# Optimization experiments

Measured on AMD Instinct MI355X. Metric: run time of the kernel, lower is better.

The kernel has to match this reference:

```python
import jax, jax.numpy as jnp
import numpy as np

METRIC = [1, 1, 1, 1, -1]  # Cl(4,1) signature (+,+,+,+,-)


def _cayley_table():
    """32x32x32 geometric-product table for Cl(4,1); exactly one nonzero per (i,j)."""
    T = np.zeros((32, 32, 32), dtype=np.float32)
    for i in range(32):
        for j in range(32):
            k = i ^ j
            sign = 1.0
            bits = [b for b in range(5) if (i >> b) & 1] + [b for b in range(5) if (j >> b) & 1]
            swaps = 0
            for _ in range(len(bits)):
                for idx in range(len(bits) - 1):
                    if bits[idx] > bits[idx + 1]:
                        bits[idx], bits[idx + 1] = bits[idx + 1], bits[idx]
                        swaps += 1
            if swaps % 2 == 1:
                sign = -sign
            common = i & j
            for b in range(5):
                if (common >> b) & 1:
                    sign *= METRIC[b]
            T[i, j, k] = sign
    return T


def _mnorm(v, eps=1e-8):
    # stabilized L2 normalization over the last (blade) axis
    return v / (jnp.linalg.norm(v, axis=-1, keepdims=True) + eps)


def setup_inputs() -> dict:
    key = jax.random.key(0)
    k1, k2, k3, k4, k5 = jax.random.split(key, 5)
    B, T, D = 128, 512, 64
    x = jax.random.randint(k1, (B, T), 0, 4)
    emb = jax.random.normal(k2, (4, 32), dtype=jnp.float32) * 0.1
    emb = emb.at[:, 0].set(1.0)  # torch init: weight[:,0] = 1
    gin = 32 + D * 32
    gate_w = jax.random.normal(k3, (D, gin), dtype=jnp.float32) / np.sqrt(gin)
    gate_b = jnp.ones((D,), dtype=jnp.float32)  # torch init: bias.fill_(1.0)
    w1 = jax.random.normal(k4, (128, D * 32), dtype=jnp.float32) / np.sqrt(D * 32)
    b1 = jnp.zeros((128,), dtype=jnp.float32)
    ln_g = jnp.ones((128,), dtype=jnp.float32)
    ln_b = jnp.zeros((128,), dtype=jnp.float32)
    w2 = jax.random.normal(k5, (2, 128), dtype=jnp.float32) / np.sqrt(128)
    b2 = jnp.zeros((2,), dtype=jnp.float32)
    gp_table = jnp.asarray(_cayley_table())
    return {"x": x, "emb": emb, "gate_w": gate_w, "gate_b": gate_b,
            "w1": w1, "b1": b1, "ln_g": ln_g, "ln_b": ln_b,
            "w2": w2, "b2": b2, "gp_table": gp_table}


def reference(x, emb, gate_w, gate_b, w1, b1, ln_g, ln_b, w2, b2, gp_table):
    B, T = x.shape
    D = gate_b.shape[0]
    r_in = _mnorm(emb[x])  # [B,T,32]
    h0 = jnp.zeros((B, D, 32), dtype=emb.dtype).at[:, :, 0].set(1.0)

    def step(h, r_t):
        # r_t: [B,32], h: [B,D,32]
        gate_in = jnp.concatenate([h.reshape(B, D * 32), r_t], axis=-1)
        g = jax.nn.sigmoid(gate_in @ gate_w.T + gate_b)[..., None]  # [B,D,1]
        h_next = jnp.einsum('bi,bdj,ijk->bdk', r_t, h, gp_table)   # geometric product
        h = _mnorm((1.0 - g) * h + g * h_next)
        return h, None

    h, _ = jax.lax.scan(step, h0, jnp.swapaxes(r_in, 0, 1))
    z = h.reshape(B, D * 32) @ w1.T + b1
    mu = jnp.mean(z, axis=-1, keepdims=True)
    var = jnp.var(z, axis=-1, keepdims=True)
    z = (z - mu) / jnp.sqrt(var + 1e-5) * ln_g + ln_b  # LayerNorm(128)
    return jax.nn.relu(z) @ w2.T + b2  # [B,2]
```

## Files before the change

kernel.cpp:

```cpp
#include <hip/hip_runtime.h>
#include <hip/hip_fp16.h>

typedef unsigned int u32;
typedef _Float16 h2f __attribute__((ext_vector_type(2)));

#define BB 128
#define TT 512
#define DD 64
#define NBL 32
#define GIN 2080

template <int CTRL>
__device__ __forceinline__ float dpp_mov_f(float x) {
  return __builtin_bit_cast(
      float, __builtin_amdgcn_update_dpp(0, __builtin_bit_cast(int, x), CTRL,
                                         0xF, 0xF, true));
}
template <int CTRL>
__device__ __forceinline__ float dpp_add_f(float x) {
  return x + dpp_mov_f<CTRL>(x);
}
__device__ __forceinline__ float4 dpp_mov_f4_x1(float4 v) {
  return make_float4(dpp_mov_f<0xB1>(v.x), dpp_mov_f<0xB1>(v.y),
                     dpp_mov_f<0xB1>(v.z), dpp_mov_f<0xB1>(v.w));
}
__device__ __forceinline__ float swz_add16(float x) {
  return x + __builtin_bit_cast(float, __builtin_amdgcn_ds_swizzle(
                                           __builtin_bit_cast(int, x), 0x401F));
}
__device__ __forceinline__ float bpermf(int addr, float x) {
  return __builtin_bit_cast(
      float, __builtin_amdgcn_ds_bpermute(addr, __builtin_bit_cast(int, x)));
}
__device__ __forceinline__ float xorf(float a, u32 m) {
  return __builtin_bit_cast(float, __builtin_bit_cast(u32, a) ^ m);
}
__device__ __forceinline__ float uni_f(float v) {
  return __builtin_bit_cast(
      float, __builtin_amdgcn_readfirstlane(__builtin_bit_cast(int, v)));
}
__device__ __forceinline__ int uni_i(int v) {
  return __builtin_amdgcn_readfirstlane(v);
}

__device__ inline int gp_negbit(int i, int j) {
  int sw = 0;
#pragma unroll
  for (int b = 0; b < 5; ++b)
    if ((j >> b) & 1) sw += __popc(i >> (b + 1));
  return (sw ^ ((i & j) >> 4)) & 1;
}

__device__ inline float fdot2f(u32 a, u32 b, float acc) {
#if __has_builtin(__builtin_amdgcn_fdot2)
  return __builtin_amdgcn_fdot2(__builtin_bit_cast(h2f, a),
                                __builtin_bit_cast(h2f, b), acc, false);
#else
  h2f av = __builtin_bit_cast(h2f, a), bv = __builtin_bit_cast(h2f, b);
  return acc + (float)av.x * (float)bv.x + (float)av.y * (float)bv.y;
#endif
}

__device__ inline u32 pkf16(float a, float b) {
  return __builtin_bit_cast(u32, __builtin_amdgcn_cvt_pkrtz(a, b));
}

#define STEP(P, RNR, XI)                                                      \
  do {                                                                        \
    const int pn = (P) ^ 1;                                                   \
            \
    const u32* Hb = &h16t[(P)][s >> 1][(s & 1) << 5];                         \
    float a0 = 0.f, a1 = 0.f, a2 = 0.f, a3 = 0.f;                             \
    _Pragma("unroll") for (int jq = 0; jq < 8; ++jq) {                        \
      uint4 hv = *(const uint4*)(Hb + (jq << 2));                             \
      a0 = fdot2f(gw[0][4 * jq + 0], hv.x, a0);                               \
      a0 = fdot2f(gw[0][4 * jq + 1], hv.y, a0);                               \
      a0 = fdot2f(gw[0][4 * jq + 2], hv.z, a0);                               \
      a0 = fdot2f(gw[0][4 * jq + 3], hv.w, a0);                               \
      a1 = fdot2f(gw[1][4 * jq + 0], hv.x, a1);                               \
      a1 = fdot2f(gw[1][4 * jq + 1], hv.y, a1);                               \
      a1 = fdot2f(gw[1][4 * jq + 2], hv.z, a1);                               \
      a1 = fdot2f(gw[1][4 * jq + 3], hv.w, a1);                               \
      a2 = fdot2f(gw[2][4 * jq + 0], hv.x, a2);                               \
      a2 = fdot2f(gw[2][4 * jq + 1], hv.y, a2);                               \
      a2 = fdot2f(gw[2][4 * jq + 2], hv.z, a2);                               \
      a2 = fdot2f(gw[2][4 * jq + 3], hv.w, a2);                               \
      a3 = fdot2f(gw[3][4 * jq + 0], hv.x, a3);                               \
      a3 = fdot2f(gw[3][4 * jq + 1], hv.y, a3);                               \
      a3 = fdot2f(gw[3][4 * jq + 2], hv.z, a3);                               \
      a3 = fdot2f(gw[3][4 * jq + 3], hv.w, a3);                               \
    }                                                                         \
    a0 = dpp_add_f<0xB1>(a0); a0 = dpp_add_f<0x4E>(a0);                       \
    a0 = dpp_add_f<0x141>(a0); a0 = dpp_add_f<0x140>(a0); a0 = swz_add16(a0); \
    a1 = dpp_add_f<0xB1>(a1); a1 = dpp_add_f<0x4E>(a1);                       \
    a1 = dpp_add_f<0x141>(a1); a1 = dpp_add_f<0x140>(a1); a1 = swz_add16(a1); \
    a2 = dpp_add_f<0xB1>(a2); a2 = dpp_add_f<0x4E>(a2);                       \
    a2 = dpp_add_f<0x141>(a2); a2 = dpp_add_f<0x140>(a2); a2 = swz_add16(a2); \
    a3 = dpp_add_f<0xB1>(a3); a3 = dpp_add_f<0x4E>(a3);                       \
    a3 = dpp_add_f<0x141>(a3); a3 = dpp_add_f<0x140>(a3); a3 = swz_add16(a3); \
    const int jsel = rl & 3;                                                  \
    float zv = (jsel == 0) ? a0 : (jsel == 1) ? a1 : (jsel == 2) ? a2 : a3;   \
    float rcsel = ((XI) == 0)   ? rcv0                                        \
                  : ((XI) == 1) ? rcv1                                        \
                  : ((XI) == 2) ? rcv2                                        \
                                : rcv3;                                       \
    float invsel = ((XI) == 0)   ? iv0                                        \
                   : ((XI) == 1) ? iv1                                        \
                   : ((XI) == 2) ? iv2                                        \
                                 : iv3;                                       \
    float g = 1.f / (1.f + exp2f(-1.44269504f * (zv + rcsel)));               \
                  \
    float4 hq[8];                                                             \
    hq[0] = make_float4(u0, u1, u2, u3);                                      \
    hq[2] = *(const float4*)&h32[(P)][d][(2 ^ c) << 2];                       \
    hq[4] = *(const float4*)&h32[(P)][d][(4 ^ c) << 2];                       \
    hq[6] = *(const float4*)&h32[(P)][d][(6 ^ c) << 2];                       \
    hq[1] = dpp_mov_f4_x1(hq[0]);                                             \
    hq[3] = dpp_mov_f4_x1(hq[2]);                                             \
    hq[5] = dpp_mov_f4_x1(hq[4]);                                             \
    hq[7] = dpp_mov_f4_x1(hq[6]);                                             \
    float b0 = 0.f, b1v = 0.f, b2v = 0.f, b3v = 0.f;                          \
    _Pragma("unroll") for (int q = 0; q < 8; ++q) {                           \
      float t0 = xorf(RNR[q], sb[q]);                                         \
      float t1 = xorf(RNR[q + 8], sb[q + 8]);                                 \
      float t2 = xorf(RNR[q + 16], sb[q + 16]);                               \
      float t3 = xorf(RNR[q + 24], sb[q + 24]);                               \
      b0 = fmaf(t0, hq[q].x, b0);                                             \
      b1v = fmaf(t0, hq[q].y, b1v);                                           \
      b2v = fmaf(t0, hq[q].z, b2v);                                           \
      b3v = fmaf(t0, hq[q].w, b3v);                                           \
      b0 = fmaf(t1, hq[q].y, b0);                                             \
      b1v = fmaf(t1, hq[q].x, b1v);                                           \
      b2v = fmaf(t1, hq[q].w, b2v);                                           \
      b3v = fmaf(t1, hq[q].z, b3v);                                           \
      b0 = fmaf(t2, hq[q].z, b0);                                             \
      b1v = fmaf(-t2, hq[q].w, b1v);                                          \
      b2v = fmaf(-t2, hq[q].x, b2v);                                          \
      b3v = fmaf(t2, hq[q].y, b3v);                                           \
      b0 = fmaf(t3, hq[q].w, b0);                                             \
      b1v = fmaf(-t3, hq[q].z, b1v);                                          \
      b2v = fmaf(-t3, hq[q].y, b2v);                                          \
      b3v = fmaf(t3, hq[q].x, b3v);                                           \
    }                                                                         \
       \
    float gi = g * invsel;                                                    \
    float om = 1.f - g;                                                       \
    float nu0 = fmaf(gi, b0, om * hq[0].x);                                   \
    float nu1 = fmaf(gi, b1v, om * hq[0].y);                                  \
    float nu2 = fmaf(gi, b2v, om * hq[0].z);                                  \
    float nu3 = fmaf(gi, b3v, om * hq[0].w);                                  \
    float sq = nu0 * nu0 + nu1 * nu1 + nu2 * nu2 + nu3 * nu3;                 \
    sq = dpp_add_f<0xB1>(sq);                                                 \
    sq = dpp_add_f<0x4E>(sq);                                                 \
    sq = dpp_add_f<0x141>(sq);                                                \
    float sc = 1.f / (sqrtf(sq) + 1e-8f);                                     \
    u0 = nu0 * sc; u1 = nu1 * sc; u2 = nu2 * sc; u3 = nu3 * sc;               \
    *(float4*)&h32[pn][d][c << 2] = make_float4(u0, u1, u2, u3);              \
    float v0 = dpp_mov_f<0xB1>(u0);                                           \
    float v1 = dpp_mov_f<0xB1>(u1);                                           \
    float v2 = dpp_mov_f<0xB1>(u2);                                           \
    float v3 = dpp_mov_f<0xB1>(u3);                                           \
    if (!(l & 1)) {                                 \
      h16t[pn][(c) >> 1][d] = pkf16(u0, v0);                                  \
      h16t[pn][(c + 8) >> 1][d] = pkf16(u1, v1);                              \
      h16t[pn][(c + 16) >> 1][d] = pkf16(u2, v2);                             \
      h16t[pn][(c + 24) >> 1][d] = pkf16(u3, v3);                             \
    }                                                                         \
    __syncthreads();                                                          \
  } while (0)

__global__ __launch_bounds__(512, 2) void versor_fused(
    const int* __restrict__ x, const float* __restrict__ emb,
    const float* __restrict__ gate_w, const float* __restrict__ gate_b,
    const float* __restrict__ w1, const float* __restrict__ b1g,
    const float* __restrict__ ln_g, const float* __restrict__ ln_b,
    const float* __restrict__ w2, const float* __restrict__ b2,
    float* __restrict__ out) {
  __shared__ float rn[4][NBL];
  __shared__ float inv_lds[4];
  __shared__ float rc[4][DD];
  __shared__ __align__(16) float h32[2][DD][36];
  __shared__ __align__(16) u32 h16t[2][16][68];
  __shared__ __align__(16) float hs[2048];
  __shared__ float redA[8][2];
  __shared__ float redB[8][2];

  const int b = blockIdx.x;
  const int tid = threadIdx.x;
  const int w = tid >> 6;
  const int l = tid & 63;
  const int rl = l >> 3;
  const int d = (w << 3) + rl;
  const int c = l & 7;
  const int r2g = l >> 5;
  const int s = l & 31;
  const int bp32 = ((l ^ 32) << 2);

  if (tid < 4) {
    float v[NBL];
    float sum = 0.f;
    for (int i = 0; i < NBL; ++i) {
      v[i] = emb[tid * NBL + i];
      sum += v[i] * v[i];
    }
    float sc = 1.f / (sqrtf(sum) + 1e-8f);
    inv_lds[tid] = sc;
    for (int i = 0; i < NBL; ++i) rn[tid][i] = v[i] * sc;
  }
  for (int idx = tid; idx < DD * 36; idx += 512) {
    int dd = idx / 36, jj = idx - dd * 36;
    h32[0][dd][jj] = (jj == 0) ? 1.f : 0.f;
  }
  for (int idx = tid; idx < 16 * 68; idx += 512) {
    int m = idx / 68, dd = idx - m * 68;
    h16t[0][m][dd] = (m == 0 && dd < 64) ? 0x00003C00u : 0u;
  }
  __syncthreads();

  if (tid < 256) {
    int e = tid >> 6, row = tid & 63;
    float sum = 0.f;
    for (int i = 0; i < NBL; ++i) sum += gate_w[row * GIN + 2048 + i] * rn[e][i];
    rc[e][row] = sum;
  }

  u32 gw[4][32];
#pragma unroll
  for (int rr = 0; rr < 4; ++rr) {
    const int row = (w << 3) + (r2g << 2) + rr;
    const float* wp = gate_w + row * GIN;
#pragma unroll
    for (int m = 0; m < 32; ++m) {
      int Dd = 32 * s + m;
      int pair = Dd >> 6, dd = Dd & 63;
      int col = dd * 32 + 2 * pair;
      gw[rr][m] = pkf16(wp[col], wp[col + 1]);
    }
  }
  const float gb = gate_b[d];

  u32 sb[NBL];
#pragma unroll
  for (int i = 0; i < NBL; ++i) sb[i] = gp_negbit(i, i ^ c) ? 0x80000000u : 0u;
  __syncthreads();

  const float rcv0 = rc[0][d] + gb, rcv1 = rc[1][d] + gb;
  const float rcv2 = rc[2][d] + gb, rcv3 = rc[3][d] + gb;
  const float iv0 = inv_lds[0], iv1 = inv_lds[1];
  const float iv2 = inv_lds[2], iv3 = inv_lds[3];

  float u0 = (c == 0) ? 1.f : 0.f, u1 = 0.f, u2 = 0.f, u3 = 0.f;

  const int* xg = x + b * TT;
  int xiA = uni_i(xg[0]);
  int xiB = uni_i(xg[1]);
  float rnA[NBL], rnB[NBL];
#pragma unroll
  for (int i = 0; i < NBL; ++i) rnA[i] = uni_f(emb[xiA * NBL + i]);

  for (int t = 0; t < TT; t += 2) {
#pragma unroll
    for (int i = 0; i < NBL; ++i) rnB[i] = uni_f(emb[xiB * NBL + i]);
    int xiC = uni_i(xg[(t + 2 < TT) ? t + 2 : 0]);
    STEP(0, rnA, xiA);
#pragma unroll
    for (int i = 0; i < NBL; ++i) rnA[i] = uni_f(emb[xiC * NBL + i]);
    int xiD = uni_i(xg[(t + 3 < TT) ? t + 3 : 0]);
    STEP(1, rnB, xiB);
    xiA = xiC;
    xiB = xiD;
  }

  {
    float* ho = hs + d * 32 + c;
    ho[0] = u0;
    ho[8] = u1;
    ho[16] = u2;
    ho[24] = u3;
  }
  __syncthreads();

  const int hr = tid >> 2;
  const int seg = tid & 3;
  float acc = 0.f;
  {
    const float4* w4 = (const float4*)(w1 + hr * 2048 + seg * 512);
    const float4* h4 = (const float4*)(hs + seg * 512);
#pragma unroll 8
    for (int k = 0; k < 128; ++k) {
      float4 a = w4[k], hv = h4[k];
      acc = fmaf(a.x, hv.x, acc);
      acc = fmaf(a.y, hv.y, acc);
      acc = fmaf(a.z, hv.z, acc);
      acc = fmaf(a.w, hv.w, acc);
    }
  }
  acc = dpp_add_f<0xB1>(acc);
  acc = dpp_add_f<0x4E>(acc);
  float z = acc + b1g[hr];

  float s1 = z, s2 = z * z;
  s1 = dpp_add_f<0xB1>(s1); s1 = dpp_add_f<0x4E>(s1);
  s1 = dpp_add_f<0x141>(s1); s1 = dpp_add_f<0x140>(s1);
  s1 = swz_add16(s1); s1 += bpermf(bp32, s1);
  s2 = dpp_add_f<0xB1>(s2); s2 = dpp_add_f<0x4E>(s2);
  s2 = dpp_add_f<0x141>(s2); s2 = dpp_add_f<0x140>(s2);
  s2 = swz_add16(s2); s2 += bpermf(bp32, s2);
  if (l == 0) { redA[w][0] = s1; redA[w][1] = s2; }
  __syncthreads();
  float tot1 = 0.f, tot2 = 0.f;
#pragma unroll
  for (int k = 0; k < 8; ++k) { tot1 += redA[k][0]; tot2 += redA[k][1]; }
  float mu = tot1 * (1.f / 512.f);
  float var = tot2 * (1.f / 512.f) - mu * mu;
  z = (z - mu) * rsqrtf(var + 1e-5f) * ln_g[hr] + ln_b[hr];
  z = fmaxf(z, 0.f);

  float c0 = (seg == 0) ? z * w2[hr] : 0.f;
  float c1 = (seg == 0) ? z * w2[128 + hr] : 0.f;
  c0 = dpp_add_f<0xB1>(c0); c0 = dpp_add_f<0x4E>(c0);
  c0 = dpp_add_f<0x141>(c0); c0 = dpp_add_f<0x140>(c0);
  c0 = swz_add16(c0); c0 += bpermf(bp32, c0);
  c1 = dpp_add_f<0xB1>(c1); c1 = dpp_add_f<0x4E>(c1);
  c1 = dpp_add_f<0x141>(c1); c1 = dpp_add_f<0x140>(c1);
  c1 = swz_add16(c1); c1 += bpermf(bp32, c1);
  if (l == 0) { redB[w][0] = c0; redB[w][1] = c1; }
  __syncthreads();
  if (tid == 0) {
    float p0 = 0.f, p1 = 0.f;
#pragma unroll
    for (int k = 0; k < 8; ++k) { p0 += redB[k][0]; p1 += redB[k][1]; }
    out[b * 2 + 0] = p0 + b2[0];
    out[b * 2 + 1] = p1 + b2[1];
  }
}

extern "C" void kernel_launch(void* const* d_in, const int* in_sizes, int n_in,
                              void* d_out, int out_size, void* d_ws,
                              size_t ws_size, hipStream_t stream) {
  (void)in_sizes; (void)n_in; (void)out_size; (void)d_ws; (void)ws_size;
  const int* x = (const int*)d_in[0];
  const float* emb = (const float*)d_in[1];
  const float* gate_w = (const float*)d_in[2];
  const float* gate_b = (const float*)d_in[3];
  const float* w1 = (const float*)d_in[4];
  const float* b1 = (const float*)d_in[5];
  const float* ln_g = (const float*)d_in[6];
  const float* ln_b = (const float*)d_in[7];
  const float* w2 = (const float*)d_in[8];
  const float* b2 = (const float*)d_in[9];
  float* out = (float*)d_out;

  versor_fused<<<dim3(BB), dim3(512), 0, stream>>>(
      x, emb, gate_w, gate_b, w1, b1, ln_g, ln_b, w2, b2, out);
}
```

Measured before the change: 846.8 us.

## Compute gate matvec with MFMA 16x16x32 f16 and cross-wave LDS reduction

Replaces the per-lane fdot2 gate matvec and its DPP/swizzle reductions with MFMA 16x16x32 f16 instructions. Each wave computes a partial sum over its 256-column slice of the hidden state, with weights pre-packed into MFMA A-fragments and h stored in a new padded f16 layout. Partials go into an LDS buffer, are summed across the 8 waves after an extra __syncthreads, and the geometric-product FMAs are interleaved with the MFMA latency. This adds a second block barrier per step and extra LDS traffic in exchange for fewer VALU instructions.

```diff
diff --git a/kernel.cpp b/kernel.cpp
--- a/kernel.cpp
+++ b/kernel.cpp
@@ -3,6 +3,8 @@
 
 typedef unsigned int u32;
 typedef _Float16 h2f __attribute__((ext_vector_type(2)));
+typedef _Float16 f16x8 __attribute__((ext_vector_type(8)));
+typedef float f32x4 __attribute__((ext_vector_type(4)));
 
 #define BB 128
 #define TT 512
@@ -51,55 +53,82 @@
   return (sw ^ ((i & j) >> 4)) & 1;
 }
 
-__device__ inline float fdot2f(u32 a, u32 b, float acc) {
-#if __has_builtin(__builtin_amdgcn_fdot2)
-  return __builtin_amdgcn_fdot2(__builtin_bit_cast(h2f, a),
-                                __builtin_bit_cast(h2f, b), acc, false);
-#else
-  h2f av = __builtin_bit_cast(h2f, a), bv = __builtin_bit_cast(h2f, b);
-  return acc + (float)av.x * (float)bv.x + (float)av.y * (float)bv.y;
-#endif
-}
-
 __device__ inline u32 pkf16(float a, float b) {
   return __builtin_bit_cast(u32, __builtin_amdgcn_cvt_pkrtz(a, b));
 }
+
+#define GPQ(Q, E, RN)                                            \
+  do {                                                           \
+    float t0 = xorf(RN[(Q)], sb[(Q)]);                           \
+    float t1 = xorf(RN[(Q) + 8], sb[(Q) + 8]);                   \
+    float t2 = xorf(RN[(Q) + 16], sb[(Q) + 16]);                 \
+    float t3 = xorf(RN[(Q) + 24], sb[(Q) + 24]);                 \
+    b0 = fmaf(t0, (E).x, b0);                                    \
+    b1v = fmaf(t0, (E).y, b1v);                                  \
+    b2v = fmaf(t0, (E).z, b2v);                                  \
+    b3v = fmaf(t0, (E).w, b3v);                                  \
+    b0 = fmaf(t1, (E).y, b0);                                    \
+    b1v = fmaf(t1, (E).x, b1v);                                  \
+    b2v = fmaf(t1, (E).w, b2v);                                  \
+    b3v = fmaf(t1, (E).z, b3v);                                  \
+    b0 = fmaf(t2, (E).z, b0);                                    \
+    b1v = fmaf(-t2, (E).w, b1v);                                 \
+    b2v = fmaf(-t2, (E).x, b2v);                                 \
+    b3v = fmaf(t2, (E).y, b3v);                                  \
+    b0 = fmaf(t3, (E).w, b0);                                    \
+    b1v = fmaf(-t3, (E).z, b1v);                                 \
+    b2v = fmaf(-t3, (E).y, b2v);                                 \
+    b3v = fmaf(t3, (E).x, b3v);                                  \
+  } while (0)
 
 #define STEP(P, RNR, XI)                                                      \
   do {                                                                        \
     const int pn = (P) ^ 1;                                                   \
-            \
-    const u32* Hb = &h16t[(P)][s >> 1][(s & 1) << 5];                         \
-    float a0 = 0.f, a1 = 0.f, a2 = 0.f, a3 = 0.f;                             \
-    _Pragma("unroll") for (int jq = 0; jq < 8; ++jq) {                        \
-      uint4 hv = *(const uint4*)(Hb + (jq << 2));                             \
-      a0 = fdot2f(gw[0][4 * jq + 0], hv.x, a0);                               \
-      a0 = fdot2f(gw[0][4 * jq + 1], hv.y, a0);                               \
-      a0 = fdot2f(gw[0][4 * jq + 2], hv.z, a0);                               \
-      a0 = fdot2f(gw[0][4 * jq + 3], hv.w, a0);                               \
-      a1 = fdot2f(gw[1][4 * jq + 0], hv.x, a1);                               \
-      a1 = fdot2f(gw[1][4 * jq + 1], hv.y, a1);                               \
-      a1 = fdot2f(gw[1][4 * jq + 2], hv.z, a1);                               \
-      a1 = fdot2f(gw[1][4 * jq + 3], hv.w, a1);                               \
-      a2 = fdot2f(gw[2][4 * jq + 0], hv.x, a2);                               \
-      a2 = fdot2f(gw[2][4 * jq + 1], hv.y, a2);                               \
-      a2 = fdot2f(gw[2][4 * jq + 2], hv.z, a2);                               \
-      a2 = fdot2f(gw[2][4 * jq + 3], hv.w, a2);                               \
-      a3 = fdot2f(gw[3][4 * jq + 0], hv.x, a3);                               \
-      a3 = fdot2f(gw[3][4 * jq + 1], hv.y, a3);                               \
-      a3 = fdot2f(gw[3][4 * jq + 2], hv.z, a3);                               \
-      a3 = fdot2f(gw[3][4 * jq + 3], hv.w, a3);                               \
+     \
+    f32x4 D0 = {0.f, 0.f, 0.f, 0.f};                                          \
+    f32x4 D1 = {0.f, 0.f, 0.f, 0.f};                                          \
+    f32x4 D2 = {0.f, 0.f, 0.f, 0.f};                                          \
+    f32x4 D3 = {0.f, 0.f, 0.f, 0.f};                                          \
+    _Pragma("unroll") for (int cc = 0; cc < 8; ++cc) {                        \
+      uint4 bv = *(const uint4*)&h16b[(P)][136 * w + 17 * cc + (g4 << 2)];    \
+      f16x8 bf = __builtin_bit_cast(f16x8, bv);                               \
+      D0 = __builtin_amdgcn_mfma_f32_16x16x32_f16(gwa[0][cc], bf, D0, 0, 0, 0); \
+      D1 = __builtin_amdgcn_mfma_f32_16x16x32_f16(gwa[1][cc], bf, D1, 0, 0, 0); \
+      D2 = __builtin_amdgcn_mfma_f32_16x16x32_f16(gwa[2][cc], bf, D2, 0, 0, 0); \
+      D3 = __builtin_amdgcn_mfma_f32_16x16x32_f16(gwa[3][cc], bf, D3, 0, 0, 0); \
     }                                                                         \
-    a0 = dpp_add_f<0xB1>(a0); a0 = dpp_add_f<0x4E>(a0);                       \
-    a0 = dpp_add_f<0x141>(a0); a0 = dpp_add_f<0x140>(a0); a0 = swz_add16(a0); \
-    a1 = dpp_add_f<0xB1>(a1); a1 = dpp_add_f<0x4E>(a1);                       \
-    a1 = dpp_add_f<0x141>(a1); a1 = dpp_add_f<0x140>(a1); a1 = swz_add16(a1); \
-    a2 = dpp_add_f<0xB1>(a2); a2 = dpp_add_f<0x4E>(a2);                       \
-    a2 = dpp_add_f<0x141>(a2); a2 = dpp_add_f<0x140>(a2); a2 = swz_add16(a2); \
-    a3 = dpp_add_f<0xB1>(a3); a3 = dpp_add_f<0x4E>(a3);                       \
-    a3 = dpp_add_f<0x141>(a3); a3 = dpp_add_f<0x140>(a3); a3 = swz_add16(a3); \
-    const int jsel = rl & 3;                                                  \
-    float zv = (jsel == 0) ? a0 : (jsel == 1) ? a1 : (jsel == 2) ? a2 : a3;   \
+     \
+    float b0 = 0.f, b1v = 0.f, b2v = 0.f, b3v = 0.f;                          \
+    {                                                                         \
+      float4 hqe = make_float4(u0, u1, u2, u3);                               \
+      float4 hqo = dpp_mov_f4_x1(hqe);                                        \
+      GPQ(0, hqe, RNR);                                                       \
+      GPQ(1, hqo, RNR);                                                       \
+      hqe = *(const float4*)&h32[(P)][d][(2 ^ cq) << 2];                      \
+      hqo = dpp_mov_f4_x1(hqe);                                               \
+      GPQ(2, hqe, RNR);                                                       \
+      GPQ(3, hqo, RNR);                                                       \
+      hqe = *(const float4*)&h32[(P)][d][(4 ^ cq) << 2];                      \
+      hqo = dpp_mov_f4_x1(hqe);                                               \
+      GPQ(4, hqe, RNR);                                                       \
+      GPQ(5, hqo, RNR);                                                       \
+      hqe = *(const float4*)&h32[(P)][d][(6 ^ cq) << 2];                      \
+      hqo = dpp_mov_f4_x1(hqe);                                               \
+      GPQ(6, hqe, RNR);                                                       \
+      GPQ(7, hqo, RNR);                                                       \
+    }                                                                         \
+          \
+    if (c16 == 0) *(float4*)&zbuf[w][(g4 << 2)] =                             \
+        make_float4(D0[0], D0[1], D0[2], D0[3]);                              \
+    if (c16 == 1) *(float4*)&zbuf[w][16 + (g4 << 2)] =                        \
+        make_float4(D1[0], D1[1], D1[2], D1[3]);                              \
+    if (c16 == 2) *(float4*)&zbuf[w][32 + (g4 << 2)] =                        \
+        make_float4(D2[0], D2[1], D2[2], D2[3]);                              \
+    if (c16 == 3) *(float4*)&zbuf[w][48 + (g4 << 2)] =                        \
+        make_float4(D3[0], D3[1], D3[2], D3[3]);                              \
+    __syncthreads();                       \
+    float zv = zbuf[0][d] + zbuf[1][d] + zbuf[2][d] + zbuf[3][d] +            \
+               zbuf[4][d] + zbuf[5][d] + zbuf[6][d] + zbuf[7][d];             \
     float rcsel = ((XI) == 0)   ? rcv0                                        \
                   : ((XI) == 1) ? rcv1                                        \
                   : ((XI) == 2) ? rcv2                                        \
@@ -109,64 +138,31 @@
                    : ((XI) == 2) ? iv2                                        \
                                  : iv3;                                       \
     float g = 1.f / (1.f + exp2f(-1.44269504f * (zv + rcsel)));               \
-                  \
-    float4 hq[8];                                                             \
-    hq[0] = make_float4(u0, u1, u2, u3);                                      \
-    hq[2] = *(const float4*)&h32[(P)][d][(2 ^ c) << 2];                       \
-    hq[4] = *(const float4*)&h32[(P)][d][(4 ^ c) << 2];                       \
-    hq[6] = *(const float4*)&h32[(P)][d][(6 ^ c) << 2];                       \
-    hq[1] = dpp_mov_f4_x1(hq[0]);                                             \
-    hq[3] = dpp_mov_f4_x1(hq[2]);                                             \
-    hq[5] = dpp_mov_f4_x1(hq[4]);                                             \
-    hq[7] = dpp_mov_f4_x1(hq[6]);                                             \
-    float b0 = 0.f, b1v = 0.f, b2v = 0.f, b3v = 0.f;                          \
-    _Pragma("unroll") for (int q = 0; q < 8; ++q) {                           \
-      float t0 = xorf(RNR[q], sb[q]);                                         \
-      float t1 = xorf(RNR[q + 8], sb[q + 8]);                                 \
-      float t2 = xorf(RNR[q + 16], sb[q + 16]);                               \
-      float t3 = xorf(RNR[q + 24], sb[q + 24]);                               \
-      b0 = fmaf(t0, hq[q].x, b0);                                             \
-      b1v = fmaf(t0, hq[q].y, b1v);                                           \
-      b2v = fmaf(t0, hq[q].z, b2v);                                           \
-      b3v = fmaf(t0, hq[q].w, b3v);                                           \
-      b0 = fmaf(t1, hq[q].y, b0);                                             \
-      b1v = fmaf(t1, hq[q].x, b1v);                                           \
-      b2v = fmaf(t1, hq[q].w, b2v);                                           \
-      b3v = fmaf(t1, hq[q].z, b3v);                                           \
-      b0 = fmaf(t2, hq[q].z, b0);                                             \
-      b1v = fmaf(-t2, hq[q].w, b1v);                                          \
-      b2v = fmaf(-t2, hq[q].x, b2v);                                          \
-      b3v = fmaf(t2, hq[q].y, b3v);                                           \
-      b0 = fmaf(t3, hq[q].w, b0);                                             \
-      b1v = fmaf(-t3, hq[q].z, b1v);                                          \
-      b2v = fmaf(-t3, hq[q].y, b2v);                                          \
-      b3v = fmaf(t3, hq[q].x, b3v);                                           \
-    }                                                                         \
-       \
+         \
     float gi = g * invsel;                                                    \
     float om = 1.f - g;                                                       \
-    float nu0 = fmaf(gi, b0, om * hq[0].x);                                   \
-    float nu1 = fmaf(gi, b1v, om * hq[0].y);                                  \
-    float nu2 = fmaf(gi, b2v, om * hq[0].z);                                  \
-    float nu3 = fmaf(gi, b3v, om * hq[0].w);                                  \
+    float nu0 = fmaf(gi, b0, om * u0);                                        \
+    float nu1 = fmaf(gi, b1v, om * u1);                                       \
+    float nu2 = fmaf(gi, b2v, om * u2);                                       \
+    float nu3 = fmaf(gi, b3v, om * u3);                                       \
     float sq = nu0 * nu0 + nu1 * nu1 + nu2 * nu2 + nu3 * nu3;                 \
     sq = dpp_add_f<0xB1>(sq);                                                 \
     sq = dpp_add_f<0x4E>(sq);                                                 \
     sq = dpp_add_f<0x141>(sq);                                                \
     float sc = 1.f / (sqrtf(sq) + 1e-8f);                                     \
     u0 = nu0 * sc; u1 = nu1 * sc; u2 = nu2 * sc; u3 = nu3 * sc;               \
-    *(float4*)&h32[pn][d][c << 2] = make_float4(u0, u1, u2, u3);              \
+    *(float4*)&h32[pn][d][cq << 2] = make_float4(u0, u1, u2, u3);             \
     float v0 = dpp_mov_f<0xB1>(u0);                                           \
     float v1 = dpp_mov_f<0xB1>(u1);                                           \
     float v2 = dpp_mov_f<0xB1>(u2);                                           \
     float v3 = dpp_mov_f<0xB1>(u3);                                           \
-    if (!(l & 1)) {                                 \
-      h16t[pn][(c) >> 1][d] = pkf16(u0, v0);                                  \
-      h16t[pn][(c + 8) >> 1][d] = pkf16(u1, v1);                              \
-      h16t[pn][(c + 16) >> 1][d] = pkf16(u2, v2);                             \
-      h16t[pn][(c + 24) >> 1][d] = pkf16(u3, v3);                             \
+    if (!(l & 1)) {             \
+      h16b[pn][17 * d + (cq >> 1)] = pkf16(u0, v0);                           \
+      h16b[pn][17 * d + (cq >> 1) + 4] = pkf16(u1, v1);                       \
+      h16b[pn][17 * d + (cq >> 1) + 8] = pkf16(u2, v2);                       \
+      h16b[pn][17 * d + (cq >> 1) + 12] = pkf16(u3, v3);                      \
     }                                                                         \
-    __syncthreads();                                                          \
+    __syncthreads();              \
   } while (0)
 
 __global__ __launch_bounds__(512, 2) void versor_fused(
@@ -180,7 +176,8 @@
   __shared__ float inv_lds[4];
   __shared__ float rc[4][DD];
   __shared__ __align__(16) float h32[2][DD][36];
-  __shared__ __align__(16) u32 h16t[2][16][68];
+  __shared__ __align__(16) u32 h16b[2][1088];
+  __shared__ float zbuf[8][DD];
   __shared__ __align__(16) float hs[2048];
   __shared__ float redA[8][2];
   __shared__ float redB[8][2];
@@ -191,9 +188,9 @@
   const int l = tid & 63;
   const int rl = l >> 3;
   const int d = (w << 3) + rl;
-  const int c = l & 7;
-  const int r2g = l >> 5;
-  const int s = l & 31;
+  const int cq = l & 7;
+  const int c16 = l & 15;
+  const int g4 = l >> 4;
   const int bp32 = ((l ^ 32) << 2);
 
   if (tid < 4) {
@@ -211,9 +208,9 @@
     int dd = idx / 36, jj = idx - dd * 36;
     h32[0][dd][jj] = (jj == 0) ? 1.f : 0.f;
   }
-  for (int idx = tid; idx < 16 * 68; idx += 512) {
-    int m = idx / 68, dd = idx - m * 68;
-    h16t[0][m][dd] = (m == 0 && dd < 64) ? 0x00003C00u : 0u;
+  for (int idx = tid; idx < 1088; idx += 512) {
+    int jj = idx - (idx / 17) * 17;
+    h16b[0][idx] = (jj == 0) ? 0x00003C00u : 0u;
   }
   __syncthreads();
 
@@ -224,24 +221,24 @@
     rc[e][row] = sum;
   }
 
-  u32 gw[4][32];
-#pragma unroll
-  for (int rr = 0; rr < 4; ++rr) {
-    const int row = (w << 3) + (r2g << 2) + rr;
-    const float* wp = gate_w + row * GIN;
-#pragma unroll
-    for (int m = 0; m < 32; ++m) {
-      int Dd = 32 * s + m;
-      int pair = Dd >> 6, dd = Dd & 63;
-      int col = dd * 32 + 2 * pair;
-      gw[rr][m] = pkf16(wp[col], wp[col + 1]);
+  f16x8 gwa[4][8];
+#pragma unroll
+  for (int t = 0; t < 4; ++t) {
+#pragma unroll
+    for (int cc = 0; cc < 8; ++cc) {
+      const float* wp =
+          gate_w + (16 * t + c16) * GIN + 256 * w + 32 * cc + 8 * g4;
+      uint4 q = make_uint4(pkf16(wp[0], wp[1]), pkf16(wp[2], wp[3]),
+                           pkf16(wp[4], wp[5]), pkf16(wp[6], wp[7]));
+      gwa[t][cc] = __builtin_bit_cast(f16x8, q);
     }
   }
   const float gb = gate_b[d];
 
   u32 sb[NBL];
 #pragma unroll
-  for (int i = 0; i < NBL; ++i) sb[i] = gp_negbit(i, i ^ c) ? 0x80000000u : 0u;
+  for (int i = 0; i < NBL; ++i)
+    sb[i] = gp_negbit(i, i ^ cq) ? 0x80000000u : 0u;
   __syncthreads();
 
   const float rcv0 = rc[0][d] + gb, rcv1 = rc[1][d] + gb;
@@ -249,7 +246,7 @@
   const float iv0 = inv_lds[0], iv1 = inv_lds[1];
   const float iv2 = inv_lds[2], iv3 = inv_lds[3];
 
-  float u0 = (c == 0) ? 1.f : 0.f, u1 = 0.f, u2 = 0.f, u3 = 0.f;
+  float u0 = (cq == 0) ? 1.f : 0.f, u1 = 0.f, u2 = 0.f, u3 = 0.f;
 
   const int* xg = x + b * TT;
   int xiA = uni_i(xg[0]);
@@ -272,7 +269,7 @@
   }
 
   {
-    float* ho = hs + d * 32 + c;
+    float* ho = hs + d * 32 + cq;
     ho[0] = u0;
     ho[8] = u1;
     ho[16] = u2;
```

Result: slower. 921.9 us (+8.9%).
